# Performance work log

Measured on AMD Instinct MI355X. Metric: run time of the kernel, lower is better.

## Reference

```python
import jax, jax.numpy as jnp
import numpy as np

NEG_INF = -1e30  # mask value used by QANet's apply_mask


def setup_inputs() -> dict:
    key = jax.random.key(0)
    ks = jax.random.split(key, 6)
    B, C, Q, H = 64, 1024, 128, 512
    return {
        "x_context": jax.random.normal(ks[0], (B, C, H), dtype=jnp.float32),
        "x_query": jax.random.normal(ks[1], (B, Q, H), dtype=jnp.float32),
        "context_mask": jnp.ones((B, C), dtype=jnp.float32),
        "query_mask": jnp.ones((B, Q), dtype=jnp.float32),
        "W0": jax.random.normal(ks[2], (H,), dtype=jnp.float32) * 0.05,
        "W1": jax.random.normal(ks[3], (H,), dtype=jnp.float32) * 0.05,
        "W2": jax.random.normal(ks[4], (H,), dtype=jnp.float32) * 0.05,
        "bias": jnp.zeros((1,), dtype=jnp.float32),
    }


def reference(x_context, x_query, context_mask, query_mask, W0, W1, W2, bias):
    # Trilinear similarity S[b,c,q] = q.W0 + c.W1 + (q*W2).c + bias
    # (original computes [B,Q,C] then transposes; we build [B,C,Q] directly)
    sub0 = jnp.einsum('bqh,h->bq', x_query, W0)          # [B,Q]
    sub1 = jnp.einsum('bch,h->bc', x_context, W1)        # [B,C]
    sub2 = jnp.einsum('bch,bqh->bcq', x_context, x_query * W2)  # [B,C,Q]
    S = sub2 + sub1[:, :, None] + sub0[:, None, :] + bias  # [B,C,Q]

    mq = query_mask[:, None, :]    # [B,1,Q]
    mc = context_mask[:, :, None]  # [B,C,1]

    # context-to-query: softmax over query axis, masked by query_mask
    S_ = jax.nn.softmax(S + (1.0 - mq) * NEG_INF, axis=-1)  # [B,C,Q]
    c2q = jnp.einsum('bcq,bqh->bch', S_, x_query)           # [B,C,H]

    # query-to-context: softmax over context axis, masked by context_mask
    S_c = jax.nn.softmax(S + (1.0 - mc) * NEG_INF, axis=1)  # [B,C,Q]
    S_T = jnp.swapaxes(S_c, 1, 2)                            # [B,Q,C]
    # (S_ @ S_T) @ x_context, associated as S_ @ (S_T @ x_context)
    tmp = jnp.einsum('bqc,bch->bqh', S_T, x_context)        # [B,Q,H]
    q2c = jnp.einsum('bcq,bqh->bch', S_, tmp)               # [B,C,H]
    return c2q, q2c
```

## Files before the change

kernel.cpp:

```cpp
#include <hip/hip_runtime.h>

#define BB 64
#define CC 1024
#define QQ 128
#define HH 512

typedef short bf16x8 __attribute__((ext_vector_type(8)));
typedef float f32x4 __attribute__((ext_vector_type(4)));

#define GLD16(g, l)                                                            \
    __builtin_amdgcn_global_load_lds(                                          \
        (const __attribute__((address_space(1))) unsigned int*)(g),            \
        (__attribute__((address_space(3))) unsigned int*)(l), 16, 0, 0)

__device__ __forceinline__ unsigned short f2bf(float f) {
    unsigned u = __float_as_uint(f);
    u += 0x7FFF + ((u >> 16) & 1);
    return (unsigned short)(u >> 16);
}
__device__ __forceinline__ unsigned pk2(float lo, float hi) {
    return (unsigned)f2bf(lo) | ((unsigned)f2bf(hi) << 16);
}

__global__ __launch_bounds__(256) void k_sub0(const float* __restrict__ xq,
                                              const float* __restrict__ w0,
                                              float* __restrict__ sub0,
                                              float* __restrict__ colsum) {
    if (blockIdx.x < 32) colsum[blockIdx.x * 256 + threadIdx.x] = 0.0f;
    int wave = threadIdx.x >> 6;
    int lane = threadIdx.x & 63;
    int row  = blockIdx.x * 4 + wave;
    const float* p = xq + (size_t)row * HH + lane * 8;
    float4 a0 = *(const float4*)(p);
    float4 a1 = *(const float4*)(p + 4);
    float4 b0 = *(const float4*)(w0 + lane * 8);
    float4 b1 = *(const float4*)(w0 + lane * 8 + 4);
    float s = a0.x*b0.x + a0.y*b0.y + a0.z*b0.z + a0.w*b0.w
            + a1.x*b1.x + a1.y*b1.y + a1.z*b1.z + a1.w*b1.w;
    #pragma unroll
    for (int off = 32; off; off >>= 1) s += __shfl_xor(s, off);
    if (lane == 0) sub0[row] = s;
}

__global__ __launch_bounds__(256) void k_prep(const float* __restrict__ xq,
                                              const float* __restrict__ w2,
                                              const float* __restrict__ qmask,
                                              unsigned short* __restrict__ xqw2b,
                                              unsigned short* __restrict__ xqmT) {
    int b  = blockIdx.y;
    int ht = blockIdx.x * 128;
    int tid = threadIdx.x;
    __shared__ __align__(16) unsigned short sT[128][132];

    {
        int q  = tid >> 1;
        int hh = (tid & 1) * 64;
        float qm = qmask[b * QQ + q];
        const float* xp = xq + ((size_t)b * QQ + q) * HH + ht + hh;
        unsigned short* wr = xqw2b + ((size_t)b * QQ + q) * HH + ht + hh;
        #pragma unroll
        for (int i = 0; i < 16; i++) {
            float4 v = *(const float4*)(xp + i * 4);
            float4 w = *(const float4*)(w2 + ht + hh + i * 4);
            uint2 pw; pw.x = pk2(v.x * w.x, v.y * w.y);
                      pw.y = pk2(v.z * w.z, v.w * w.w);
            *(uint2*)(wr + i * 4) = pw;
            uint2 pm; pm.x = pk2(v.x * qm, v.y * qm);
                      pm.y = pk2(v.z * qm, v.w * qm);
            *(uint2*)(&sT[q][hh + i * 4]) = pm;
        }
    }
    __syncthreads();
    {
        int h  = tid >> 1;
        int qh = (tid & 1) * 64;
        unsigned short* orow = xqmT + ((size_t)b * HH + ht + h) * QQ + qh;
        #pragma unroll
        for (int i = 0; i < 8; i++) {
            uint4 o;
            o.x = (unsigned)sT[qh + i*8 + 0][h] | ((unsigned)sT[qh + i*8 + 1][h] << 16);
            o.y = (unsigned)sT[qh + i*8 + 2][h] | ((unsigned)sT[qh + i*8 + 3][h] << 16);
            o.z = (unsigned)sT[qh + i*8 + 4][h] | ((unsigned)sT[qh + i*8 + 5][h] << 16);
            o.w = (unsigned)sT[qh + i*8 + 6][h] | ((unsigned)sT[qh + i*8 + 7][h] << 16);
            *(uint4*)(orow + i * 8) = o;
        }
    }
}

__global__ __launch_bounds__(256) void k_scores(
    const float* __restrict__ xc, const unsigned short* __restrict__ xqw2b,
    const float* __restrict__ w1, const float* __restrict__ cmask,
    const float* __restrict__ qmask, const float* __restrict__ bias,
    const float* __restrict__ sub0, unsigned short* __restrict__ Ebf,
    float* __restrict__ rowsum, float* __restrict__ colsum) {
    int b  = blockIdx.y;
    int c0 = blockIdx.x * 128;
    int tid  = threadIdx.x;
    int lane = tid & 63, wave = tid >> 6;
    int quad = lane >> 4, lcol = lane & 15;
    int wrow = (wave >> 1) * 64, wcol = (wave & 1) * 64;

    __shared__ __align__(16) unsigned short sA[2][128][32];
    __shared__ __align__(16) unsigned short sB[2][128][32];
    __shared__ float sW1[512];
    __shared__ float sSub1[128];
    __shared__ float sS0[128], sQm[128], sCm[128];
    __shared__ float sRowP[2][128], sColP[2][128];

    sW1[tid] = w1[tid]; sW1[tid + 256] = w1[tid + 256];
    if (tid < 128) {
        sS0[tid] = sub0[b * QQ + tid] + bias[0];
        sQm[tid] = qmask[b * QQ + tid];
        sCm[tid] = cmask[b * CC + c0 + tid];
    }

    f32x4 acc[4][4];
    #pragma unroll
    for (int i = 0; i < 4; i++)
        #pragma unroll
        for (int j = 0; j < 4; j++) acc[i][j] = (f32x4)0.0f;
    float s1 = 0.0f;

    int arow = tid >> 1, akh = (tid & 1) * 16;
    const float* gbase = xc + ((size_t)(b * CC + c0 + arow)) * HH + akh;

    __syncthreads();

    {
        float4 v0 = *(const float4*)(gbase);
        float4 v1 = *(const float4*)(gbase + 4);
        float4 v2 = *(const float4*)(gbase + 8);
        float4 v3 = *(const float4*)(gbase + 12);
        const float* wp = sW1 + akh;
        s1 += v0.x*wp[0] + v0.y*wp[1] + v0.z*wp[2] + v0.w*wp[3]
            + v1.x*wp[4] + v1.y*wp[5] + v1.z*wp[6] + v1.w*wp[7]
            + v2.x*wp[8] + v2.y*wp[9] + v2.z*wp[10] + v2.w*wp[11]
            + v3.x*wp[12] + v3.y*wp[13] + v3.z*wp[14] + v3.w*wp[15];
        uint4 p0, p1;
        p0.x = pk2(v0.x, v0.y); p0.y = pk2(v0.z, v0.w);
        p0.z = pk2(v1.x, v1.y); p0.w = pk2(v1.z, v1.w);
        p1.x = pk2(v2.x, v2.y); p1.y = pk2(v2.z, v2.w);
        p1.z = pk2(v3.x, v3.y); p1.w = pk2(v3.z, v3.w);
        *(uint4*)&sA[0][arow][akh]     = p0;
        *(uint4*)&sA[0][arow][akh + 8] = p1;
    }
    #pragma unroll
    for (int j = 0; j < 2; j++) {
        int chunk = wave * 2 + j;
        int row = chunk * 16 + (lane >> 2);
        GLD16(xqw2b + ((size_t)b * QQ + row) * HH + (lane & 3) * 8,
              (unsigned short*)sB[0] + chunk * 512);
    }
    __syncthreads();

    for (int t = 0; t < 16; ++t) {
        int cur = t & 1, alt = cur ^ 1;
        bool pf = (t < 15);
        int kn = (t + 1) * 32;
        float4 v0, v1, v2, v3;
        if (pf) {
            const float* gp = gbase + kn;
            v0 = *(const float4*)(gp);
            v1 = *(const float4*)(gp + 4);
            v2 = *(const float4*)(gp + 8);
            v3 = *(const float4*)(gp + 12);
            #pragma unroll
            for (int j = 0; j < 2; j++) {
                int chunk = wave * 2 + j;
                int row = chunk * 16 + (lane >> 2);
                GLD16(xqw2b + ((size_t)b * QQ + row) * HH + kn + (lane & 3) * 8,
                      (unsigned short*)sB[alt] + chunk * 512);
            }
        }
        bf16x8 af[4];
        #pragma unroll
        for (int mi = 0; mi < 4; mi++)
            af[mi] = *(const bf16x8*)&sA[cur][wrow + mi * 16 + lcol][quad * 8];
        #pragma unroll
        for (int ni = 0; ni < 4; ni++) {
            bf16x8 bfr = *(const bf16x8*)&sB[cur][wcol + ni * 16 + lcol][quad * 8];
            #pragma unroll
            for (int mi = 0; mi < 4; mi++)
                acc[mi][ni] = __builtin_amdgcn_mfma_f32_16x16x32_bf16(
                    af[mi], bfr, acc[mi][ni], 0, 0, 0);
        }
        if (pf) {
            const float* wp = sW1 + kn + akh;
            s1 += v0.x*wp[0] + v0.y*wp[1] + v0.z*wp[2] + v0.w*wp[3]
                + v1.x*wp[4] + v1.y*wp[5] + v1.z*wp[6] + v1.w*wp[7]
                + v2.x*wp[8] + v2.y*wp[9] + v2.z*wp[10] + v2.w*wp[11]
                + v3.x*wp[12] + v3.y*wp[13] + v3.z*wp[14] + v3.w*wp[15];
            uint4 p0, p1;
            p0.x = pk2(v0.x, v0.y); p0.y = pk2(v0.z, v0.w);
            p0.z = pk2(v1.x, v1.y); p0.w = pk2(v1.z, v1.w);
            p1.x = pk2(v2.x, v2.y); p1.y = pk2(v2.z, v2.w);
            p1.z = pk2(v3.x, v3.y); p1.w = pk2(v3.z, v3.w);
            *(uint4*)&sA[alt][arow][akh]     = p0;
            *(uint4*)&sA[alt][arow][akh + 8] = p1;
        }
        __syncthreads();
    }

    s1 += __shfl_xor(s1, 1);
    if ((tid & 1) == 0) sSub1[arow] = s1;
    __syncthreads();

    float rsp[4][4];
    float csp[4] = {0.f, 0.f, 0.f, 0.f};
    #pragma unroll
    for (int mi = 0; mi < 4; mi++)
        #pragma unroll
        for (int r = 0; r < 4; r++) rsp[mi][r] = 0.f;

    #pragma unroll
    for (int mi = 0; mi < 4; mi++) {
        #pragma unroll
        for (int ni = 0; ni < 4; ni++) {
            int col = wcol + ni * 16 + lcol;
            float qm = sQm[col], s0 = sS0[col];
            #pragma unroll
            for (int r = 0; r < 4; r++) {
                int row = wrow + mi * 16 + quad * 4 + r;
                float e = __expf(acc[mi][ni][r] + sSub1[row] + s0);
                acc[mi][ni][r] = e;
                rsp[mi][r] += e * qm;
                csp[ni] += e * sCm[row];
            }
        }
    }
    #pragma unroll
    for (int mi = 0; mi < 4; mi++)
        #pragma unroll
        for (int r = 0; r < 4; r++) {
            float v = rsp[mi][r];
            v += __shfl_xor(v, 1); v += __shfl_xor(v, 2);
            v += __shfl_xor(v, 4); v += __shfl_xor(v, 8);
            if (lcol == 0) sRowP[wave & 1][wrow + mi * 16 + quad * 4 + r] = v;
        }
    #pragma unroll
    for (int ni = 0; ni < 4; ni++) {
        float v = csp[ni];
        v += __shfl_xor(v, 16); v += __shfl_xor(v, 32);
        if (quad == 0) sColP[wave >> 1][wcol + ni * 16 + lcol] = v;
    }
    #pragma unroll
    for (int mi = 0; mi < 4; mi++)
        #pragma unroll
        for (int ni = 0; ni < 4; ni++) {
            int col = wcol + ni * 16 + lcol;
            #pragma unroll
            for (int r = 0; r < 4; r++) {
                int row = wrow + mi * 16 + quad * 4 + r;
                Ebf[((size_t)(b * CC + c0 + row)) * QQ + col] = f2bf(acc[mi][ni][r]);
            }
        }
    __syncthreads();
    if (tid < 128) {
        rowsum[(size_t)b * CC + c0 + tid] = sRowP[0][tid] + sRowP[1][tid];
        atomicAdd(&colsum[b * QQ + tid], sColP[0][tid] + sColP[1][tid]);
    }
}

__global__ __launch_bounds__(256) void k_tmp(
    const unsigned short* __restrict__ Ebf, const float* __restrict__ xc,
    const float* __restrict__ cmask, const float* __restrict__ qmask,
    const float* __restrict__ colsum, unsigned short* __restrict__ tmpT) {
    int b  = blockIdx.y;
    int h0 = blockIdx.x * 64;
    int tid  = threadIdx.x;
    int lane = tid & 63, wave = tid >> 6;
    int quad = lane >> 4, lcol = lane & 15;
    int wrow = (wave >> 1) * 64;
    int wcol = (wave & 1) * 32;

    __shared__ __align__(16) unsigned int sAu[2][128 * 16];
    __shared__ __align__(16) unsigned int sBu[2][64 * 16];
    __shared__ float sInv[128];
    if (tid < 128) sInv[tid] = qmask[b * QQ + tid] / colsum[b * QQ + tid];

    f32x4 acc[4][2];
    #pragma unroll
    for (int i = 0; i < 4; i++) { acc[i][0] = (f32x4)0.f; acc[i][1] = (f32x4)0.f; }

    int tp = tid >> 4;
    int tq = tid & 15;

    const unsigned short* ebase = Ebf + ((size_t)b * CC + 2 * tp) * QQ + tq * 8;
    const float*          xbase = xc  + ((size_t)b * CC + 2 * tp) * HH + h0 + tq * 4;
    const float*          mbase = cmask + (size_t)b * CC + 2 * tp;

    {
        union { uint4 v; unsigned short s[8]; } r0, r1;
        r0.v = *(const uint4*)(ebase);
        r1.v = *(const uint4*)(ebase + QQ);
        float cm0 = mbase[0];
        float cm1 = mbase[1];
        float4 f0 = *(const float4*)(xbase);
        float4 f1 = *(const float4*)(xbase + HH);
        #pragma unroll
        for (int j = 0; j < 8; j++) {
            int q = tq * 8 + j;
            unsigned pk = (unsigned)r0.s[j] | ((unsigned)r1.s[j] << 16);
            sAu[0][q * 16 + (((tp >> 2) ^ (q >> 3 & 3)) << 2) + (tp & 3)] = pk;
        }
        float a0[4] = {f0.x, f0.y, f0.z, f0.w};
        float a1[4] = {f1.x, f1.y, f1.z, f1.w};
        #pragma unroll
        for (int j = 0; j < 4; j++) {
            int h = tq * 4 + j;
            unsigned pk = pk2(a0[j] * cm0, a1[j] * cm1);
            sBu[0][h * 16 + (((tp >> 2) ^ (h >> 3 & 3)) << 2) + (tp & 3)] = pk;
        }
    }
    __syncthreads();

    for (int t = 0; t < 32; ++t) {
        int cur = t & 1, alt = cur ^ 1;
        bool pf = (t < 31);
        int cn = (t + 1) * 32;
        union { uint4 v; unsigned short s[8]; } r0, r1;
        float4 f0, f1;
        float cm0, cm1;
        if (pf) {
            r0.v = *(const uint4*)(ebase + (size_t)cn * QQ);
            r1.v = *(const uint4*)(ebase + (size_t)cn * QQ + QQ);
            cm0 = mbase[cn];
            cm1 = mbase[cn + 1];
            f0 = *(const float4*)(xbase + (size_t)cn * HH);
            f1 = *(const float4*)(xbase + (size_t)cn * HH + HH);
        }
        bf16x8 af[4];
        #pragma unroll
        for (int mi = 0; mi < 4; mi++) {
            int m = wrow + mi * 16 + lcol;
            af[mi] = *(const bf16x8*)(sAu[cur] + m * 16 + ((quad ^ (m >> 3 & 3)) << 2));
        }
        #pragma unroll
        for (int ni = 0; ni < 2; ni++) {
            int n = wcol + ni * 16 + lcol;
            bf16x8 bfr = *(const bf16x8*)(sBu[cur] + n * 16 + ((quad ^ (n >> 3 & 3)) << 2));
            #pragma unroll
            for (int mi = 0; mi < 4; mi++)
                acc[mi][ni] = __builtin_amdgcn_mfma_f32_16x16x32_bf16(
                    af[mi], bfr, acc[mi][ni], 0, 0, 0);
        }
        if (pf) {
            #pragma unroll
            for (int j = 0; j < 8; j++) {
                int q = tq * 8 + j;
                unsigned pk = (unsigned)r0.s[j] | ((unsigned)r1.s[j] << 16);
                sAu[alt][q * 16 + (((tp >> 2) ^ (q >> 3 & 3)) << 2) + (tp & 3)] = pk;
            }
            float a0[4] = {f0.x, f0.y, f0.z, f0.w};
            float a1[4] = {f1.x, f1.y, f1.z, f1.w};
            #pragma unroll
            for (int j = 0; j < 4; j++) {
                int h = tq * 4 + j;
                unsigned pk = pk2(a0[j] * cm0, a1[j] * cm1);
                sBu[alt][h * 16 + (((tp >> 2) ^ (h >> 3 & 3)) << 2) + (tp & 3)] = pk;
            }
        }
        __syncthreads();
    }
    #pragma unroll
    for (int mi = 0; mi < 4; mi++) {
        int qb = wrow + mi * 16 + quad * 4;
        #pragma unroll
        for (int ni = 0; ni < 2; ni++) {
            int h = wcol + ni * 16 + lcol;
            uint2 o;
            o.x = pk2(acc[mi][ni][0] * sInv[qb + 0], acc[mi][ni][1] * sInv[qb + 1]);
            o.y = pk2(acc[mi][ni][2] * sInv[qb + 2], acc[mi][ni][3] * sInv[qb + 3]);
            *(uint2*)(tmpT + ((size_t)b * HH + h0 + h) * QQ + qb) = o;
        }
    }
}

__global__ __launch_bounds__(256) void k_out(
    const unsigned short* __restrict__ Ebf, const unsigned short* __restrict__ xqmT,
    const unsigned short* __restrict__ tmpT, const float* __restrict__ rowsum,
    float* __restrict__ c2q, float* __restrict__ q2c) {
    int b  = blockIdx.z;
    int c0 = blockIdx.y * 128;
    int h0 = blockIdx.x * 128;
    int tid  = threadIdx.x;
    int lane = tid & 63, wave = tid >> 6;
    int quad = lane >> 4, lcol = lane & 15;
    int wrow = (wave >> 1) * 64, wcol = (wave & 1) * 64;

    __shared__ __align__(16) unsigned short sA[2][128][32];
    __shared__ __align__(16) unsigned short sB1[2][128][32];
    __shared__ __align__(16) unsigned short sB2[2][128][32];
    __shared__ float sInvR[128];
    if (tid < 128) sInvR[tid] = 1.0f / rowsum[(size_t)b * CC + c0 + tid];

    f32x4 acc1[4][4], acc2[4][4];
    #pragma unroll
    for (int i = 0; i < 4; i++)
        #pragma unroll
        for (int j = 0; j < 4; j++) { acc1[i][j] = (f32x4)0.f; acc2[i][j] = (f32x4)0.f; }

    #pragma unroll
    for (int j = 0; j < 2; j++) {
        int chunk = wave * 2 + j;
        int row = chunk * 16 + (lane >> 2);
        int kb  = (lane & 3) * 8;
        GLD16(Ebf  + ((size_t)b * CC + c0 + row) * QQ + kb,
              (unsigned short*)sA[0] + chunk * 512);
        GLD16(xqmT + ((size_t)b * HH + h0 + row) * QQ + kb,
              (unsigned short*)sB1[0] + chunk * 512);
        GLD16(tmpT + ((size_t)b * HH + h0 + row) * QQ + kb,
              (unsigned short*)sB2[0] + chunk * 512);
    }
    __syncthreads();

    for (int t = 0; t < 4; ++t) {
        int cur = t & 1, alt = cur ^ 1;
        bool pf = (t < 3);
        int kn = (t + 1) * 32;
        if (pf) {
            #pragma unroll
            for (int j = 0; j < 2; j++) {
                int chunk = wave * 2 + j;
                int row = chunk * 16 + (lane >> 2);
                int kb  = (lane & 3) * 8;
                GLD16(Ebf  + ((size_t)b * CC + c0 + row) * QQ + kn + kb,
                      (unsigned short*)sA[alt] + chunk * 512);
                GLD16(xqmT + ((size_t)b * HH + h0 + row) * QQ + kn + kb,
                      (unsigned short*)sB1[alt] + chunk * 512);
                GLD16(tmpT + ((size_t)b * HH + h0 + row) * QQ + kn + kb,
                      (unsigned short*)sB2[alt] + chunk * 512);
            }
        }
        bf16x8 af[4];
        #pragma unroll
        for (int mi = 0; mi < 4; mi++)
            af[mi] = *(const bf16x8*)&sA[cur][wrow + mi * 16 + lcol][quad * 8];
        #pragma unroll
        for (int ni = 0; ni < 4; ni++) {
            bf16x8 b1 = *(const bf16x8*)&sB1[cur][wcol + ni * 16 + lcol][quad * 8];
            bf16x8 b2 = *(const bf16x8*)&sB2[cur][wcol + ni * 16 + lcol][quad * 8];
            #pragma unroll
            for (int mi = 0; mi < 4; mi++) {
                acc1[mi][ni] = __builtin_amdgcn_mfma_f32_16x16x32_bf16(
                    af[mi], b1, acc1[mi][ni], 0, 0, 0);
                acc2[mi][ni] = __builtin_amdgcn_mfma_f32_16x16x32_bf16(
                    af[mi], b2, acc2[mi][ni], 0, 0, 0);
            }
        }
        __syncthreads();
    }
    #pragma unroll
    for (int mi = 0; mi < 4; mi++) {
        int rb = wrow + mi * 16 + quad * 4;
        float ir0 = sInvR[rb], ir1 = sInvR[rb + 1], ir2 = sInvR[rb + 2], ir3 = sInvR[rb + 3];
        #pragma unroll
        for (int ni = 0; ni < 4; ni++) {
            int col = h0 + wcol + ni * 16 + lcol;
            size_t o0 = ((size_t)b * CC + c0 + rb) * HH + col;
            c2q[o0]          = acc1[mi][ni][0] * ir0;
            c2q[o0 + HH]     = acc1[mi][ni][1] * ir1;
            c2q[o0 + 2*HH]   = acc1[mi][ni][2] * ir2;
            c2q[o0 + 3*HH]   = acc1[mi][ni][3] * ir3;
            q2c[o0]          = acc2[mi][ni][0] * ir0;
            q2c[o0 + HH]     = acc2[mi][ni][1] * ir1;
            q2c[o0 + 2*HH]   = acc2[mi][ni][2] * ir2;
            q2c[o0 + 3*HH]   = acc2[mi][ni][3] * ir3;
        }
    }
}

extern "C" void kernel_launch(void* const* d_in, const int* in_sizes, int n_in,
                              void* d_out, int out_size, void* d_ws, size_t ws_size,
                              hipStream_t stream) {
    const float* xc    = (const float*)d_in[0];
    const float* xq    = (const float*)d_in[1];
    const float* cmask = (const float*)d_in[2];
    const float* qmask = (const float*)d_in[3];
    const float* w0    = (const float*)d_in[4];
    const float* w1    = (const float*)d_in[5];
    const float* w2    = (const float*)d_in[6];
    const float* bias  = (const float*)d_in[7];

    float* out = (float*)d_out;
    float* c2q = out;
    float* q2c = out + (size_t)BB * CC * HH;

    unsigned short* Ebf   = (unsigned short*)d_ws;
    unsigned short* xqw2b = Ebf   + (size_t)BB * CC * QQ;
    unsigned short* xqmT  = xqw2b + (size_t)BB * QQ * HH;
    unsigned short* tmpT  = xqmT  + (size_t)BB * QQ * HH;
    float* rowsum = (float*)(tmpT + (size_t)BB * QQ * HH);
    float* colsum = rowsum + (size_t)BB * CC;
    float* sub0   = colsum + (size_t)BB * QQ;

    k_sub0  <<<dim3(BB * QQ / 4),      256, 0, stream>>>(xq, w0, sub0, colsum);
    k_prep  <<<dim3(HH / 128, BB),     256, 0, stream>>>(xq, w2, qmask, xqw2b, xqmT);
    k_scores<<<dim3(CC / 128, BB),     256, 0, stream>>>(xc, xqw2b, w1, cmask, qmask,
                                                         bias, sub0, Ebf, rowsum, colsum);
    k_tmp   <<<dim3(HH / 64, BB),      256, 0, stream>>>(Ebf, xc, cmask, qmask,
                                                         colsum, tmpT);
    k_out   <<<dim3(HH / 128, CC / 128, BB), 256, 0, stream>>>(Ebf, xqmT, tmpT,
                                                               rowsum, c2q, q2c);
}
```

Measured before the change: 483.7 us.

## Split score, tmp and output kernels into smaller tiles for more blocks

The score kernel now handles 64 context rows per block instead of 128, the tmp kernel splits the query dimension across two blocks, and the output kernel computes c2q and q2c in separate blocks rather than sharing the A tile between two accumulator sets. This doubles grid sizes and halves per-block accumulator and LDS use, aiming for more occupancy and better load balance across CUs. In exchange, the Ebf A tile is loaded twice in the output kernel, the xqw2b B tile is read by twice as many score blocks, and the colsum atomics double.

```diff
diff --git a/kernel.cpp b/kernel.cpp
--- a/kernel.cpp
+++ b/kernel.cpp
@@ -94,34 +94,34 @@
     const float* __restrict__ sub0, unsigned short* __restrict__ Ebf,
     float* __restrict__ rowsum, float* __restrict__ colsum) {
     int b  = blockIdx.y;
-    int c0 = blockIdx.x * 128;
+    int c0 = blockIdx.x * 64;
     int tid  = threadIdx.x;
     int lane = tid & 63, wave = tid >> 6;
     int quad = lane >> 4, lcol = lane & 15;
-    int wrow = (wave >> 1) * 64, wcol = (wave & 1) * 64;
-
-    __shared__ __align__(16) unsigned short sA[2][128][32];
+    int wrow = (wave >> 1) * 32, wcol = (wave & 1) * 64;
+
+    __shared__ __align__(16) unsigned short sA[2][64][32];
     __shared__ __align__(16) unsigned short sB[2][128][32];
     __shared__ float sW1[512];
-    __shared__ float sSub1[128];
-    __shared__ float sS0[128], sQm[128], sCm[128];
-    __shared__ float sRowP[2][128], sColP[2][128];
+    __shared__ float sSub1[64];
+    __shared__ float sS0[128], sQm[128], sCm[64];
+    __shared__ float sRowP[2][64], sColP[2][128];
 
     sW1[tid] = w1[tid]; sW1[tid + 256] = w1[tid + 256];
     if (tid < 128) {
         sS0[tid] = sub0[b * QQ + tid] + bias[0];
         sQm[tid] = qmask[b * QQ + tid];
-        sCm[tid] = cmask[b * CC + c0 + tid];
-    }
-
-    f32x4 acc[4][4];
-    #pragma unroll
-    for (int i = 0; i < 4; i++)
+    }
+    if (tid < 64) sCm[tid] = cmask[b * CC + c0 + tid];
+
+    f32x4 acc[2][4];
+    #pragma unroll
+    for (int i = 0; i < 2; i++)
         #pragma unroll
         for (int j = 0; j < 4; j++) acc[i][j] = (f32x4)0.0f;
     float s1 = 0.0f;
 
-    int arow = tid >> 1, akh = (tid & 1) * 16;
+    int arow = tid >> 2, akh = (tid & 3) * 8;
     const float* gbase = xc + ((size_t)(b * CC + c0 + arow)) * HH + akh;
 
     __syncthreads();
@@ -129,20 +129,13 @@
     {
         float4 v0 = *(const float4*)(gbase);
         float4 v1 = *(const float4*)(gbase + 4);
-        float4 v2 = *(const float4*)(gbase + 8);
-        float4 v3 = *(const float4*)(gbase + 12);
         const float* wp = sW1 + akh;
         s1 += v0.x*wp[0] + v0.y*wp[1] + v0.z*wp[2] + v0.w*wp[3]
-            + v1.x*wp[4] + v1.y*wp[5] + v1.z*wp[6] + v1.w*wp[7]
-            + v2.x*wp[8] + v2.y*wp[9] + v2.z*wp[10] + v2.w*wp[11]
-            + v3.x*wp[12] + v3.y*wp[13] + v3.z*wp[14] + v3.w*wp[15];
-        uint4 p0, p1;
-        p0.x = pk2(v0.x, v0.y); p0.y = pk2(v0.z, v0.w);
-        p0.z = pk2(v1.x, v1.y); p0.w = pk2(v1.z, v1.w);
-        p1.x = pk2(v2.x, v2.y); p1.y = pk2(v2.z, v2.w);
-        p1.z = pk2(v3.x, v3.y); p1.w = pk2(v3.z, v3.w);
-        *(uint4*)&sA[0][arow][akh]     = p0;
-        *(uint4*)&sA[0][arow][akh + 8] = p1;
+            + v1.x*wp[4] + v1.y*wp[5] + v1.z*wp[6] + v1.w*wp[7];
+        uint4 p;
+        p.x = pk2(v0.x, v0.y); p.y = pk2(v0.z, v0.w);
+        p.z = pk2(v1.x, v1.y); p.w = pk2(v1.z, v1.w);
+        *(uint4*)&sA[0][arow][akh] = p;
     }
     #pragma unroll
     for (int j = 0; j < 2; j++) {
@@ -157,13 +150,11 @@
         int cur = t & 1, alt = cur ^ 1;
         bool pf = (t < 15);
         int kn = (t + 1) * 32;
-        float4 v0, v1, v2, v3;
+        float4 v0, v1;
         if (pf) {
             const float* gp = gbase + kn;
             v0 = *(const float4*)(gp);
             v1 = *(const float4*)(gp + 4);
-            v2 = *(const float4*)(gp + 8);
-            v3 = *(const float4*)(gp + 12);
             #pragma unroll
             for (int j = 0; j < 2; j++) {
                 int chunk = wave * 2 + j;
@@ -172,48 +163,44 @@
                       (unsigned short*)sB[alt] + chunk * 512);
             }
         }
-        bf16x8 af[4];
-        #pragma unroll
-        for (int mi = 0; mi < 4; mi++)
+        bf16x8 af[2];
+        #pragma unroll
+        for (int mi = 0; mi < 2; mi++)
             af[mi] = *(const bf16x8*)&sA[cur][wrow + mi * 16 + lcol][quad * 8];
         #pragma unroll
         for (int ni = 0; ni < 4; ni++) {
             bf16x8 bfr = *(const bf16x8*)&sB[cur][wcol + ni * 16 + lcol][quad * 8];
             #pragma unroll
-            for (int mi = 0; mi < 4; mi++)
+            for (int mi = 0; mi < 2; mi++)
                 acc[mi][ni] = __builtin_amdgcn_mfma_f32_16x16x32_bf16(
                     af[mi], bfr, acc[mi][ni], 0, 0, 0);
         }
         if (pf) {
             const float* wp = sW1 + kn + akh;
             s1 += v0.x*wp[0] + v0.y*wp[1] + v0.z*wp[2] + v0.w*wp[3]
-                + v1.x*wp[4] + v1.y*wp[5] + v1.z*wp[6] + v1.w*wp[7]
-                + v2.x*wp[8] + v2.y*wp[9] + v2.z*wp[10] + v2.w*wp[11]
-                + v3.x*wp[12] + v3.y*wp[13] + v3.z*wp[14] + v3.w*wp[15];
-            uint4 p0, p1;
-            p0.x = pk2(v0.x, v0.y); p0.y = pk2(v0.z, v0.w);
-            p0.z = pk2(v1.x, v1.y); p0.w = pk2(v1.z, v1.w);
-            p1.x = pk2(v2.x, v2.y); p1.y = pk2(v2.z, v2.w);
-            p1.z = pk2(v3.x, v3.y); p1.w = pk2(v3.z, v3.w);
-            *(uint4*)&sA[alt][arow][akh]     = p0;
-            *(uint4*)&sA[alt][arow][akh + 8] = p1;
+                + v1.x*wp[4] + v1.y*wp[5] + v1.z*wp[6] + v1.w*wp[7];
+            uint4 p;
+            p.x = pk2(v0.x, v0.y); p.y = pk2(v0.z, v0.w);
+            p.z = pk2(v1.x, v1.y); p.w = pk2(v1.z, v1.w);
+            *(uint4*)&sA[alt][arow][akh] = p;
         }
         __syncthreads();
     }
 
     s1 += __shfl_xor(s1, 1);
-    if ((tid & 1) == 0) sSub1[arow] = s1;
-    __syncthreads();
-
-    float rsp[4][4];
+    s1 += __shfl_xor(s1, 2);
+    if ((tid & 3) == 0) sSub1[arow] = s1;
+    __syncthreads();
+
+    float rsp[2][4];
     float csp[4] = {0.f, 0.f, 0.f, 0.f};
     #pragma unroll
-    for (int mi = 0; mi < 4; mi++)
+    for (int mi = 0; mi < 2; mi++)
         #pragma unroll
         for (int r = 0; r < 4; r++) rsp[mi][r] = 0.f;
 
     #pragma unroll
-    for (int mi = 0; mi < 4; mi++) {
+    for (int mi = 0; mi < 2; mi++) {
         #pragma unroll
         for (int ni = 0; ni < 4; ni++) {
             int col = wcol + ni * 16 + lcol;
@@ -229,7 +216,7 @@
         }
     }
     #pragma unroll
-    for (int mi = 0; mi < 4; mi++)
+    for (int mi = 0; mi < 2; mi++)
         #pragma unroll
         for (int r = 0; r < 4; r++) {
             float v = rsp[mi][r];
@@ -244,7 +231,7 @@
         if (quad == 0) sColP[wave >> 1][wcol + ni * 16 + lcol] = v;
     }
     #pragma unroll
-    for (int mi = 0; mi < 4; mi++)
+    for (int mi = 0; mi < 2; mi++)
         #pragma unroll
         for (int ni = 0; ni < 4; ni++) {
             int col = wcol + ni * 16 + lcol;
@@ -255,10 +242,10 @@
             }
         }
     __syncthreads();
-    if (tid < 128) {
+    if (tid < 64)
         rowsum[(size_t)b * CC + c0 + tid] = sRowP[0][tid] + sRowP[1][tid];
+    if (tid < 128)
         atomicAdd(&colsum[b * QQ + tid], sColP[0][tid] + sColP[1][tid]);
-    }
 }
 
 __global__ __launch_bounds__(256) void k_tmp(
@@ -266,40 +253,41 @@
     const float* __restrict__ cmask, const float* __restrict__ qmask,
     const float* __restrict__ colsum, unsigned short* __restrict__ tmpT) {
     int b  = blockIdx.y;
-    int h0 = blockIdx.x * 64;
+    int h0 = (blockIdx.x >> 1) * 64;
+    int q0 = (blockIdx.x & 1) * 64;
     int tid  = threadIdx.x;
     int lane = tid & 63, wave = tid >> 6;
     int quad = lane >> 4, lcol = lane & 15;
-    int wrow = (wave >> 1) * 64;
+    int wrow = (wave >> 1) * 32;
     int wcol = (wave & 1) * 32;
 
-    __shared__ __align__(16) unsigned int sAu[2][128 * 16];
+    __shared__ __align__(16) unsigned int sAu[2][64 * 16];
     __shared__ __align__(16) unsigned int sBu[2][64 * 16];
-    __shared__ float sInv[128];
-    if (tid < 128) sInv[tid] = qmask[b * QQ + tid] / colsum[b * QQ + tid];
-
-    f32x4 acc[4][2];
-    #pragma unroll
-    for (int i = 0; i < 4; i++) { acc[i][0] = (f32x4)0.f; acc[i][1] = (f32x4)0.f; }
+    __shared__ float sInv[64];
+    if (tid < 64) sInv[tid] = qmask[b * QQ + q0 + tid] / colsum[b * QQ + q0 + tid];
+
+    f32x4 acc[2][2];
+    #pragma unroll
+    for (int i = 0; i < 2; i++) { acc[i][0] = (f32x4)0.f; acc[i][1] = (f32x4)0.f; }
 
     int tp = tid >> 4;
     int tq = tid & 15;
 
-    const unsigned short* ebase = Ebf + ((size_t)b * CC + 2 * tp) * QQ + tq * 8;
+    const unsigned short* ebase = Ebf + ((size_t)b * CC + 2 * tp) * QQ + q0 + tq * 4;
     const float*          xbase = xc  + ((size_t)b * CC + 2 * tp) * HH + h0 + tq * 4;
     const float*          mbase = cmask + (size_t)b * CC + 2 * tp;
 
     {
-        union { uint4 v; unsigned short s[8]; } r0, r1;
-        r0.v = *(const uint4*)(ebase);
-        r1.v = *(const uint4*)(ebase + QQ);
+        union { uint2 v; unsigned short s[4]; } r0, r1;
+        r0.v = *(const uint2*)(ebase);
+        r1.v = *(const uint2*)(ebase + QQ);
         float cm0 = mbase[0];
         float cm1 = mbase[1];
         float4 f0 = *(const float4*)(xbase);
         float4 f1 = *(const float4*)(xbase + HH);
         #pragma unroll
-        for (int j = 0; j < 8; j++) {
-            int q = tq * 8 + j;
+        for (int j = 0; j < 4; j++) {
+            int q = tq * 4 + j;
             unsigned pk = (unsigned)r0.s[j] | ((unsigned)r1.s[j] << 16);
             sAu[0][q * 16 + (((tp >> 2) ^ (q >> 3 & 3)) << 2) + (tp & 3)] = pk;
         }
@@ -318,20 +306,20 @@
         int cur = t & 1, alt = cur ^ 1;
         bool pf = (t < 31);
         int cn = (t + 1) * 32;
-        union { uint4 v; unsigned short s[8]; } r0, r1;
+        union { uint2 v; unsigned short s[4]; } r0, r1;
         float4 f0, f1;
         float cm0, cm1;
         if (pf) {
-            r0.v = *(const uint4*)(ebase + (size_t)cn * QQ);
-            r1.v = *(const uint4*)(ebase + (size_t)cn * QQ + QQ);
+            r0.v = *(const uint2*)(ebase + (size_t)cn * QQ);
+            r1.v = *(const uint2*)(ebase + (size_t)cn * QQ + QQ);
             cm0 = mbase[cn];
             cm1 = mbase[cn + 1];
             f0 = *(const float4*)(xbase + (size_t)cn * HH);
             f1 = *(const float4*)(xbase + (size_t)cn * HH + HH);
         }
-        bf16x8 af[4];
-        #pragma unroll
-        for (int mi = 0; mi < 4; mi++) {
+        bf16x8 af[2];
+        #pragma unroll
+        for (int mi = 0; mi < 2; mi++) {
             int m = wrow + mi * 16 + lcol;
             af[mi] = *(const bf16x8*)(sAu[cur] + m * 16 + ((quad ^ (m >> 3 & 3)) << 2));
         }
@@ -340,14 +328,14 @@
             int n = wcol + ni * 16 + lcol;
             bf16x8 bfr = *(const bf16x8*)(sBu[cur] + n * 16 + ((quad ^ (n >> 3 & 3)) << 2));
             #pragma unroll
-            for (int mi = 0; mi < 4; mi++)
+            for (int mi = 0; mi < 2; mi++)
                 acc[mi][ni] = __builtin_amdgcn_mfma_f32_16x16x32_bf16(
                     af[mi], bfr, acc[mi][ni], 0, 0, 0);
         }
         if (pf) {
             #pragma unroll
-            for (int j = 0; j < 8; j++) {
-                int q = tq * 8 + j;
+            for (int j = 0; j < 4; j++) {
+                int q = tq * 4 + j;
                 unsigned pk = (unsigned)r0.s[j] | ((unsigned)r1.s[j] << 16);
                 sAu[alt][q * 16 + (((tp >> 2) ^ (q >> 3 & 3)) << 2) + (tp & 3)] = pk;
             }
@@ -363,7 +351,7 @@
         __syncthreads();
     }
     #pragma unroll
-    for (int mi = 0; mi < 4; mi++) {
+    for (int mi = 0; mi < 2; mi++) {
         int qb = wrow + mi * 16 + quad * 4;
         #pragma unroll
         for (int ni = 0; ni < 2; ni++) {
@@ -371,7 +359,7 @@
             uint2 o;
             o.x = pk2(acc[mi][ni][0] * sInv[qb + 0], acc[mi][ni][1] * sInv[qb + 1]);
             o.y = pk2(acc[mi][ni][2] * sInv[qb + 2], acc[mi][ni][3] * sInv[qb + 3]);
-            *(uint2*)(tmpT + ((size_t)b * HH + h0 + h) * QQ + qb) = o;
+            *(uint2*)(tmpT + ((size_t)b * HH + h0 + h) * QQ + q0 + qb) = o;
         }
     }
 }
@@ -382,23 +370,25 @@
     float* __restrict__ c2q, float* __restrict__ q2c) {
     int b  = blockIdx.z;
     int c0 = blockIdx.y * 128;
-    int h0 = blockIdx.x * 128;
+    int which = blockIdx.x & 1;
+    int h0 = (blockIdx.x >> 1) * 128;
+    const unsigned short* Bsrc = which ? tmpT : xqmT;
+    float* dst = which ? q2c : c2q;
     int tid  = threadIdx.x;
     int lane = tid & 63, wave = tid >> 6;
     int quad = lane >> 4, lcol = lane & 15;
     int wrow = (wave >> 1) * 64, wcol = (wave & 1) * 64;
 
     __shared__ __align__(16) unsigned short sA[2][128][32];
-    __shared__ __align__(16) unsigned short sB1[2][128][32];
-    __shared__ __align__(16) unsigned short sB2[2][128][32];
+    __shared__ __align__(16) unsigned short sB[2][128][32];
     __shared__ float sInvR[128];
     if (tid < 128) sInvR[tid] = 1.0f / rowsum[(size_t)b * CC + c0 + tid];
 
-    f32x4 acc1[4][4], acc2[4][4];
+    f32x4 acc[4][4];
     #pragma unroll
     for (int i = 0; i < 4; i++)
         #pragma unroll
-        for (int j = 0; j < 4; j++) { acc1[i][j] = (f32x4)0.f; acc2[i][j] = (f32x4)0.f; }
+        for (int j = 0; j < 4; j++) acc[i][j] = (f32x4)0.f;
 
     #pragma unroll
     for (int j = 0; j < 2; j++) {
@@ -407,10 +397,8 @@
         int kb  = (lane & 3) * 8;
         GLD16(Ebf  + ((size_t)b * CC + c0 + row) * QQ + kb,
               (unsigned short*)sA[0] + chunk * 512);
-        GLD16(xqmT + ((size_t)b * HH + h0 + row) * QQ + kb,
-              (unsigned short*)sB1[0] + chunk * 512);
-        GLD16(tmpT + ((size_t)b * HH + h0 + row) * QQ + kb,
-              (unsigned short*)sB2[0] + chunk * 512);
+        GLD16(Bsrc + ((size_t)b * HH + h0 + row) * QQ + kb,
+              (unsigned short*)sB[0] + chunk * 512);
     }
     __syncthreads();
 
@@ -426,10 +414,8 @@
                 int kb  = (lane & 3) * 8;
                 GLD16(Ebf  + ((size_t)b * CC + c0 + row) * QQ + kn + kb,
                       (unsigned short*)sA[alt] + chunk * 512);
-                GLD16(xqmT + ((size_t)b * HH + h0 + row) * QQ + kn + kb,
-                      (unsigned short*)sB1[alt] + chunk * 512);
-                GLD16(tmpT + ((size_t)b * HH + h0 + row) * QQ + kn + kb,
-                      (unsigned short*)sB2[alt] + chunk * 512);
+                GLD16(Bsrc + ((size_t)b * HH + h0 + row) * QQ + kn + kb,
+                      (unsigned short*)sB[alt] + chunk * 512);
             }
         }
         bf16x8 af[4];
@@ -438,15 +424,11 @@
             af[mi] = *(const bf16x8*)&sA[cur][wrow + mi * 16 + lcol][quad * 8];
         #pragma unroll
         for (int ni = 0; ni < 4; ni++) {
-            bf16x8 b1 = *(const bf16x8*)&sB1[cur][wcol + ni * 16 + lcol][quad * 8];
-            bf16x8 b2 = *(const bf16x8*)&sB2[cur][wcol + ni * 16 + lcol][quad * 8];
-            #pragma unroll
-            for (int mi = 0; mi < 4; mi++) {
-                acc1[mi][ni] = __builtin_amdgcn_mfma_f32_16x16x32_bf16(
-                    af[mi], b1, acc1[mi][ni], 0, 0, 0);
-                acc2[mi][ni] = __builtin_amdgcn_mfma_f32_16x16x32_bf16(
-                    af[mi], b2, acc2[mi][ni], 0, 0, 0);
-            }
+            bf16x8 bfr = *(const bf16x8*)&sB[cur][wcol + ni * 16 + lcol][quad * 8];
+            #pragma unroll
+            for (int mi = 0; mi < 4; mi++)
+                acc[mi][ni] = __builtin_amdgcn_mfma_f32_16x16x32_bf16(
+                    af[mi], bfr, acc[mi][ni], 0, 0, 0);
         }
         __syncthreads();
     }
@@ -458,14 +440,10 @@
         for (int ni = 0; ni < 4; ni++) {
             int col = h0 + wcol + ni * 16 + lcol;
             size_t o0 = ((size_t)b * CC + c0 + rb) * HH + col;
-            c2q[o0]          = acc1[mi][ni][0] * ir0;
-            c2q[o0 + HH]     = acc1[mi][ni][1] * ir1;
-            c2q[o0 + 2*HH]   = acc1[mi][ni][2] * ir2;
-            c2q[o0 + 3*HH]   = acc1[mi][ni][3] * ir3;
-            q2c[o0]          = acc2[mi][ni][0] * ir0;
-            q2c[o0 + HH]     = acc2[mi][ni][1] * ir1;
-            q2c[o0 + 2*HH]   = acc2[mi][ni][2] * ir2;
-            q2c[o0 + 3*HH]   = acc2[mi][ni][3] * ir3;
+            dst[o0]          = acc[mi][ni][0] * ir0;
+            dst[o0 + HH]     = acc[mi][ni][1] * ir1;
+            dst[o0 + 2*HH]   = acc[mi][ni][2] * ir2;
+            dst[o0 + 3*HH]   = acc[mi][ni][3] * ir3;
         }
     }
 }
@@ -494,12 +472,12 @@
     float* colsum = rowsum + (size_t)BB * CC;
     float* sub0   = colsum + (size_t)BB * QQ;
 
-    k_sub0  <<<dim3(BB * QQ / 4),      256, 0, stream>>>(xq, w0, sub0, colsum);
-    k_prep  <<<dim3(HH / 128, BB),     256, 0, stream>>>(xq, w2, qmask, xqw2b, xqmT);
-    k_scores<<<dim3(CC / 128, BB),     256, 0, stream>>>(xc, xqw2b, w1, cmask, qmask,
-                                                         bias, sub0, Ebf, rowsum, colsum);
-    k_tmp   <<<dim3(HH / 64, BB),      256, 0, stream>>>(Ebf, xc, cmask, qmask,
-                                                         colsum, tmpT);
-    k_out   <<<dim3(HH / 128, CC / 128, BB), 256, 0, stream>>>(Ebf, xqmT, tmpT,
-                                                               rowsum, c2q, q2c);
-}
+    k_sub0  <<<dim3(BB * QQ / 4),          256, 0, stream>>>(xq, w0, sub0, colsum);
+    k_prep  <<<dim3(HH / 128, BB),         256, 0, stream>>>(xq, w2, qmask, xqw2b, xqmT);
+    k_scores<<<dim3(CC / 64, BB),          256, 0, stream>>>(xc, xqw2b, w1, cmask, qmask,
+                                                             bias, sub0, Ebf, rowsum, colsum);
+    k_tmp   <<<dim3((HH / 64) * 2, BB),    256, 0, stream>>>(Ebf, xc, cmask, qmask,
+                                                             colsum, tmpT);
+    k_out   <<<dim3((HH / 128) * 2, CC / 128, BB), 256, 0, stream>>>(Ebf, xqmT, tmpT,
+                                                                     rowsum, c2q, q2c);
+}
```

Result: no change. 491.0 us (+1.5%).
